# Kernel tuning notes

Measured on AMD Instinct MI355X. Metric: run time of the kernel, lower is better.

## Reference

```python
import jax, jax.numpy as jnp
import numpy as np

T = 4096          # total tokens across ragged segments
H = 4096          # hidden_size
I = 11008         # intermediate_size
R = 16            # lora_rank
A = 4             # number of adapters (segments)


def setup_inputs() -> dict:
    key = jax.random.key(0)
    ks = jax.random.split(key, 12)
    inp = {
        "x": jax.random.normal(ks[0], (T, H), jnp.float32),
        "gate_w": jax.random.normal(ks[1], (I, H), jnp.float32) * (1.0 / np.sqrt(H)),
        "up_w": jax.random.normal(ks[2], (I, H), jnp.float32) * (1.0 / np.sqrt(H)),
        "down_w": jax.random.normal(ks[3], (H, I), jnp.float32) * (1.0 / np.sqrt(I)),
        "gate_wa": jax.random.normal(ks[4], (A, H, R), jnp.float32) * 0.01,
        "gate_wb": jax.random.normal(ks[5], (A, R, I), jnp.float32) * 0.01,
        "up_wa": jax.random.normal(ks[6], (A, H, R), jnp.float32) * 0.01,
        "up_wb": jax.random.normal(ks[7], (A, R, I), jnp.float32) * 0.01,
        "down_wa": jax.random.normal(ks[8], (A, I, R), jnp.float32) * 0.01,
        "down_wb": jax.random.normal(ks[9], (A, R, H), jnp.float32) * 0.01,
        "seg_ids": jnp.sort(jax.random.randint(ks[10], (T,), 0, A, jnp.int32)),
    }
    return inp


def _add_lora(y, inp, wa, wb, mask):
    # Segment-batched low-rank GEMM (Punica/S-LoRA add_lora):
    # for token t in segment a:  y[t] += inp[t] @ wa[a] @ wb[a]
    # mask: [T, A] one-hot of token->adapter assignment.
    # [A, T, R]: project into rank space for every adapter (R tiny), mask out
    xa = jnp.einsum('th,ahr->tar', inp, wa) * mask[:, :, None]   # [T, A, R]
    a, r = wb.shape[0], wb.shape[1]
    # collapse (A, R) so the expansion is one GEMM, no [A, T, out] intermediate
    delta = xa.reshape(inp.shape[0], a * r) @ wb.reshape(a * r, wb.shape[2])
    return y + delta


def reference(x, gate_w, up_w, down_w, gate_wa, gate_wb, up_wa, up_wb,
              down_wa, down_wb, seg_ids):
    mask = (seg_ids[:, None] == jnp.arange(A, dtype=seg_ids.dtype)[None, :]
            ).astype(x.dtype)                                    # [T, A]
    gate = x @ gate_w.T                                          # [T, I]
    gate = _add_lora(gate, x, gate_wa, gate_wb, mask)
    gate = jax.nn.silu(gate)
    up = x @ up_w.T                                              # [T, I]
    up = _add_lora(up, x, up_wa, up_wb, mask)
    t = gate * up
    down = t @ down_w.T                                          # [T, H]
    down = _add_lora(down, t, down_wa, down_wb, mask)
    return down
```

## Files before the change

kernel.cpp:

```cpp
#include <hip/hip_runtime.h>

#define T_TOK 4096
#define HID   4096
#define IMD   11008

using f32x4  = __attribute__((ext_vector_type(4))) float;
using bf16x8 = __attribute__((ext_vector_type(8))) __bf16;
union FragCast { int4 i; bf16x8 b; };

__device__ __forceinline__ unsigned f2bf_bits(float f) {
  unsigned u = __float_as_uint(f);
  return (u + 0x7fffu + ((u >> 16) & 1u)) >> 16;
}
__device__ __forceinline__ float bf2f(short s) {
  return __uint_as_float(((unsigned)(unsigned short)s) << 16);
}
__device__ __forceinline__ int4 cvt8(const float4 f0, const float4 f1) {
  int4 r;
  r.x = f2bf_bits(f0.x) | (f2bf_bits(f0.y) << 16);
  r.y = f2bf_bits(f0.z) | (f2bf_bits(f0.w) << 16);
  r.z = f2bf_bits(f1.x) | (f2bf_bits(f1.y) << 16);
  r.w = f2bf_bits(f1.z) | (f2bf_bits(f1.w) << 16);
  return r;
}
__device__ __forceinline__ void gload16(const void* g, void* l) {
  __builtin_amdgcn_global_load_lds(
      (__attribute__((address_space(1))) void*)g,
      (__attribute__((address_space(3))) void*)l, 16, 0, 0);
}

__global__ void cvt_pad(const float* __restrict__ in, short* __restrict__ out,
                        int C8, long ldin, long ldout) {
  long r = blockIdx.x;
  const float4* s = (const float4*)(in + r * ldin);
  int4* d = (int4*)(out + r * ldout);
  for (int c = threadIdx.x; c < C8; c += blockDim.x)
    d[c] = cvt8(s[2 * c], s[2 * c + 1]);
}

__global__ void build_wbT_pad(const float* __restrict__ wb,
                              short* __restrict__ out, int N, long ldout,
                              long K) {
  int n = blockIdx.x * blockDim.x + threadIdx.x;
  int ar = blockIdx.y;
  if (n < N) out[(long)n * ldout + K + ar] = (short)f2bf_bits(wb[(long)ar * N + n]);
}

__global__ void tail_copy(const short* __restrict__ src, short* dst, long ld) {
  dst[(long)blockIdx.x * ld + threadIdx.x] = src[blockIdx.x * 64 + threadIdx.x];
}

template <int KD, int NOUT>
__global__ __launch_bounds__(256)
void lora_proj(const short* __restrict__ Abf, long ldA,
               const float* __restrict__ wa0, const float* __restrict__ wa1,
               const int* __restrict__ seg, short* out0, long ld0, short* out1,
               long ld1) {
  __shared__ __align__(16) short rowbuf[KD];
  __shared__ float part[NOUT][4][16];
  int t = blockIdx.x, tid = threadIdx.x;
  int a = seg[t];
  const int4* src = (const int4*)(Abf + (long)t * ldA);
  for (int c = tid; c < KD / 8; c += 256) ((int4*)rowbuf)[c] = src[c];
  __syncthreads();
  int w = tid >> 6, l = tid & 63;
  int r = l & 15, g = l >> 4;
  const int HW = KD / 4;
  float s0 = 0.f, s1 = 0.f;
  const float* p0 = wa0 + (long)a * KD * 16 + r;
  const float* p1 = (NOUT == 2) ? (wa1 + (long)a * KD * 16 + r) : nullptr;
  int h = w * HW + g;
  for (int k = 0; k < HW / 4; ++k, h += 4) {
    float xv = bf2f(rowbuf[h]);
    s0 = fmaf(xv, p0[(long)h * 16], s0);
    if (NOUT == 2) s1 = fmaf(xv, p1[(long)h * 16], s1);
  }
  s0 += __shfl_xor(s0, 16); s0 += __shfl_xor(s0, 32);
  if (NOUT == 2) { s1 += __shfl_xor(s1, 16); s1 += __shfl_xor(s1, 32); }
  if (l < 16) { part[0][w][r] = s0; if (NOUT == 2) part[1][w][r] = s1; }
  __syncthreads();
  if (tid < 64 * NOUT) {
    int m = tid >> 6, ar = tid & 63;
    float v = 0.f;
    if ((ar >> 4) == a) {
      int r2 = ar & 15;
      v = part[m][0][r2] + part[m][1][r2] + part[m][2][r2] + part[m][3][r2];
    }
    short b = (short)f2bf_bits(v);
    if (m == 0) out0[(long)t * ld0 + ar] = b;
    else        out1[(long)t * ld1 + ar] = b;
  }
}

template <int MODE>
__global__ __launch_bounds__(512, 2)
void gemm256(const short* __restrict__ A, const short* __restrict__ B,
             const short* gbuf, short* outB, float* outF, int nby, long ldK,
             int iters, long ldo) {
  extern __shared__ __align__(16) char smem[];

  int nwg = gridDim.x;
  int orig = blockIdx.x;
  int q = nwg >> 3, rr = nwg & 7;
  int xcd = orig & 7, loc = orig >> 3;
  int swz = (xcd < rr ? xcd * (q + 1) : rr * (q + 1) + (xcd - rr) * q) + loc;
  int by = swz % nby, bx = swz / nby;
  long row0 = (long)bx * 256, col0 = (long)by * 256;

  int tid = threadIdx.x;
  int l = tid & 63, wid = tid >> 6;
  int wr = wid >> 2, wc = wid & 3;
  int lrow = l & 15, lhi = l >> 4, md = lrow & 7;

  const short* aP[4]; const short* bP[4];
  int dst[4];
#pragma unroll
  for (int k = 0; k < 4; ++k) {
    int idx = tid + k * 512;
    int r = idx >> 3, c8 = idx & 7;
    aP[k] = A + (row0 + r) * ldK + (c8 ^ (r & 7)) * 8;
    bP[k] = B + (col0 + r) * ldK + (c8 ^ (r & 7)) * 8;
    dst[k] = idx * 16;
  }

  auto stageA = [&](int bi) {
    char* d = smem + bi * 32768;
#pragma unroll
    for (int k = 0; k < 4; ++k) { gload16(aP[k], d + dst[k]); aP[k] += 64; }
  };
  auto stageB = [&](int bi) {
    char* d = smem + 98304 + bi * 32768;
#pragma unroll
    for (int k = 0; k < 4; ++k) { gload16(bP[k], d + dst[k]); bP[k] += 64; }
  };

  f32x4 acc[8][4];
  f32x4 zr = {0.f, 0.f, 0.f, 0.f};
#pragma unroll
  for (int mi = 0; mi < 8; ++mi)
#pragma unroll
    for (int ni = 0; ni < 4; ++ni) acc[mi][ni] = zr;

  const int csel0 = (lhi ^ md) * 16;
  const int csel1 = ((4 + lhi) ^ md) * 16;

  stageA(0); stageB(0); stageA(1);
  int ca = 0, sa = 2;
  for (int t = 0; t < iters; ++t) {
    if (t + 1 < iters) asm volatile("s_waitcnt vmcnt(4)" ::: "memory");
    else               asm volatile("s_waitcnt vmcnt(0)" ::: "memory");
    asm volatile("s_barrier" ::: "memory");
    if (t + 1 < iters) stageB((t + 1) & 1);
    if (t + 2 < iters) { stageA(sa); sa = (sa == 2) ? 0 : sa + 1; }

    const char* Ab = smem + ca * 32768;
    const char* Bb = smem + 98304 + (t & 1) * 32768;
    ca = (ca == 2) ? 0 : ca + 1;

    bf16x8 bF[4][2];
#pragma unroll
    for (int ni = 0; ni < 4; ++ni) {
      const char* base = Bb + (wc * 64 + ni * 16 + lrow) * 128;
      FragCast f0, f1;
      f0.i = *(const int4*)(base + csel0);
      f1.i = *(const int4*)(base + csel1);
      bF[ni][0] = f0.b; bF[ni][1] = f1.b;
    }
#pragma unroll
    for (int qm = 0; qm < 2; ++qm) {
      bf16x8 aF[4][2];
#pragma unroll
      for (int mi = 0; mi < 4; ++mi) {
        const char* base = Ab + (wr * 128 + qm * 64 + mi * 16 + lrow) * 128;
        FragCast f0, f1;
        f0.i = *(const int4*)(base + csel0);
        f1.i = *(const int4*)(base + csel1);
        aF[mi][0] = f0.b; aF[mi][1] = f1.b;
      }
      __builtin_amdgcn_s_setprio(1);
#pragma unroll
      for (int mi = 0; mi < 4; ++mi)
#pragma unroll
        for (int ni = 0; ni < 4; ++ni) {
          acc[qm * 4 + mi][ni] = __builtin_amdgcn_mfma_f32_16x16x32_bf16(
              aF[mi][0], bF[ni][0], acc[qm * 4 + mi][ni], 0, 0, 0);
          acc[qm * 4 + mi][ni] = __builtin_amdgcn_mfma_f32_16x16x32_bf16(
              aF[mi][1], bF[ni][1], acc[qm * 4 + mi][ni], 0, 0, 0);
        }
      __builtin_amdgcn_s_setprio(0);
    }
  }

#pragma unroll
  for (int qm = 0; qm < 2; ++qm)
#pragma unroll
    for (int mi = 0; mi < 4; ++mi)
#pragma unroll
      for (int ni = 0; ni < 4; ++ni)
#pragma unroll
        for (int j = 0; j < 4; ++j) {
          long grow = row0 + wr * 128 + qm * 64 + mi * 16 + lhi * 4 + j;
          long gcol = col0 + wc * 64 + ni * 16 + lrow;
          long idx = grow * ldo + gcol;
          float v = acc[qm * 4 + mi][ni][j];
          if constexpr (MODE == 0) {
            outB[idx] = (short)f2bf_bits(v);
          } else if constexpr (MODE == 1) {
            float g = bf2f(gbuf[idx]);
            float t2 = g * (1.f / (1.f + __expf(-g))) * v;
            outB[idx] = (short)f2bf_bits(t2);
          } else {
            outF[idx] = v;
          }
        }
}

extern "C" void kernel_launch(void* const* d_in, const int* in_sizes, int n_in,
                              void* d_out, int out_size, void* d_ws,
                              size_t ws_size, hipStream_t stream) {
  const float* x       = (const float*)d_in[0];
  const float* gate_w  = (const float*)d_in[1];
  const float* up_w    = (const float*)d_in[2];
  const float* down_w  = (const float*)d_in[3];
  const float* gate_wa = (const float*)d_in[4];
  const float* gate_wb = (const float*)d_in[5];
  const float* up_wa   = (const float*)d_in[6];
  const float* up_wb   = (const float*)d_in[7];
  const float* down_wa = (const float*)d_in[8];
  const float* down_wb = (const float*)d_in[9];
  const int*   seg     = (const int*)d_in[10];

  char* ws = (char*)d_ws;
  short* xg_pad = (short*)(ws);
  short* wA     = (short*)(ws + 34078720);
  short* wB     = (short*)(ws + 125665280);
  short* t_pad  = (short*)(ws + 217251840);
  short* xa_u   = (short*)(ws + 307953664);

  const int LDS_BYTES = 163840;
  hipFuncSetAttribute(reinterpret_cast<const void*>(&gemm256<0>),
                      hipFuncAttributeMaxDynamicSharedMemorySize, LDS_BYTES);
  hipFuncSetAttribute(reinterpret_cast<const void*>(&gemm256<1>),
                      hipFuncAttributeMaxDynamicSharedMemorySize, LDS_BYTES);
  hipFuncSetAttribute(reinterpret_cast<const void*>(&gemm256<2>),
                      hipFuncAttributeMaxDynamicSharedMemorySize, LDS_BYTES);

  cvt_pad<<<T_TOK, 256, 0, stream>>>(x, xg_pad, 512, HID, 4160);
  cvt_pad<<<IMD, 256, 0, stream>>>(gate_w, wA, 512, HID, 4160);
  cvt_pad<<<IMD, 256, 0, stream>>>(up_w, wB, 512, HID, 4160);
  build_wbT_pad<<<dim3(43, 64), 256, 0, stream>>>(gate_wb, wA, IMD, 4160, HID);
  build_wbT_pad<<<dim3(43, 64), 256, 0, stream>>>(up_wb, wB, IMD, 4160, HID);
  lora_proj<HID, 2><<<T_TOK, 256, 0, stream>>>(
      xg_pad, 4160, gate_wa, up_wa, seg, xg_pad + HID, 4160, xa_u, 64);

  gemm256<0><<<16 * 43, 512, LDS_BYTES, stream>>>(
      xg_pad, wA, nullptr, t_pad, nullptr, 43, 4160, 65, 11072);
  tail_copy<<<T_TOK, 64, 0, stream>>>(xa_u, xg_pad + HID, 4160);
  gemm256<1><<<16 * 43, 512, LDS_BYTES, stream>>>(
      xg_pad, wB, t_pad, t_pad, nullptr, 43, 4160, 65, 11072);

  cvt_pad<<<T_TOK, 256, 0, stream>>>(down_w, wA, 1376, IMD, 11072);
  build_wbT_pad<<<dim3(16, 64), 256, 0, stream>>>(down_wb, wA, HID, 11072, IMD);
  lora_proj<IMD, 1><<<T_TOK, 256, 0, stream>>>(
      t_pad, 11072, down_wa, nullptr, seg, t_pad + IMD, 11072, nullptr, 64);

  gemm256<2><<<16 * 16, 512, LDS_BYTES, stream>>>(
      t_pad, wA, nullptr, nullptr, (float*)d_out, 16, 11072, 173, 4096);
}
```

Baseline: 1.719 ms.

## Interleave global-to-LDS stage loads across four MFMA phases per K-step

Each K-iteration of the GEMM main loop is split into four phases, each handling 32 rows of the A tile. Half-tile global loads for the next B and next-next A buffers are issued between these phases, instead of all at once at the top of the iteration. Barriers are placed around each MFMA cluster so waves stay in lockstep, in the style of ping-pong scheduling. The aim is to spread memory issue across the compute and keep the MFMA pipe busy. The cost is eight barriers per iteration instead of one, which may add stalls.

```diff
diff --git a/kernel.cpp b/kernel.cpp
--- a/kernel.cpp
+++ b/kernel.cpp
@@ -123,15 +123,15 @@
     dst[k] = idx * 16;
   }
 
-  auto stageA = [&](int bi) {
+  auto stageA_h = [&](int bi, int h) {
     char* d = smem + bi * 32768;
-#pragma unroll
-    for (int k = 0; k < 4; ++k) { gload16(aP[k], d + dst[k]); aP[k] += 64; }
+    gload16(aP[2 * h], d + dst[2 * h]);         aP[2 * h] += 64;
+    gload16(aP[2 * h + 1], d + dst[2 * h + 1]); aP[2 * h + 1] += 64;
   };
-  auto stageB = [&](int bi) {
+  auto stageB_h = [&](int bi, int h) {
     char* d = smem + 98304 + bi * 32768;
-#pragma unroll
-    for (int k = 0; k < 4; ++k) { gload16(bP[k], d + dst[k]); bP[k] += 64; }
+    gload16(bP[2 * h], d + dst[2 * h]);         bP[2 * h] += 64;
+    gload16(bP[2 * h + 1], d + dst[2 * h + 1]); bP[2 * h + 1] += 64;
   };
 
   f32x4 acc[8][4];
@@ -144,75 +144,88 @@
   const int csel0 = (lhi ^ md) * 16;
   const int csel1 = ((4 + lhi) ^ md) * 16;
 
-  stageA(0); stageB(0); stageA(1);
-  int ca = 0, sa = 2;
+  stageA_h(0, 0); stageA_h(0, 1);
+  stageB_h(0, 0); stageB_h(0, 1);
+  stageA_h(1, 0); stageA_h(1, 1);
+  asm volatile("s_waitcnt vmcnt(4)" ::: "memory");
+  asm volatile("s_barrier" ::: "memory");
+
+  int ca = 0;
   for (int t = 0; t < iters; ++t) {
-    if (t + 1 < iters) asm volatile("s_waitcnt vmcnt(4)" ::: "memory");
-    else               asm volatile("s_waitcnt vmcnt(0)" ::: "memory");
-    asm volatile("s_barrier" ::: "memory");
-    if (t + 1 < iters) stageB((t + 1) & 1);
-    if (t + 2 < iters) { stageA(sa); sa = (sa == 2) ? 0 : sa + 1; }
-
     const char* Ab = smem + ca * 32768;
     const char* Bb = smem + 98304 + (t & 1) * 32768;
-    ca = (ca == 2) ? 0 : ca + 1;
-
+    int na2 = (ca >= 1) ? ca - 1 : 2;
+    int nb1 = (t + 1) & 1;
     bf16x8 bF[4][2];
-#pragma unroll
-    for (int ni = 0; ni < 4; ++ni) {
-      const char* base = Bb + (wc * 64 + ni * 16 + lrow) * 128;
-      FragCast f0, f1;
-      f0.i = *(const int4*)(base + csel0);
-      f1.i = *(const int4*)(base + csel1);
-      bF[ni][0] = f0.b; bF[ni][1] = f1.b;
-    }
-#pragma unroll
-    for (int qm = 0; qm < 2; ++qm) {
-      bf16x8 aF[4][2];
-#pragma unroll
-      for (int mi = 0; mi < 4; ++mi) {
-        const char* base = Ab + (wr * 128 + qm * 64 + mi * 16 + lrow) * 128;
+
+#pragma unroll
+    for (int p = 0; p < 4; ++p) {
+      if (p == 0) {
+#pragma unroll
+        for (int ni = 0; ni < 4; ++ni) {
+          const char* base = Bb + (wc * 64 + ni * 16 + lrow) * 128;
+          FragCast f0, f1;
+          f0.i = *(const int4*)(base + csel0);
+          f1.i = *(const int4*)(base + csel1);
+          bF[ni][0] = f0.b; bF[ni][1] = f1.b;
+        }
+      }
+      bf16x8 aF[2][2];
+#pragma unroll
+      for (int m2 = 0; m2 < 2; ++m2) {
+        const char* base = Ab + (wr * 128 + p * 32 + m2 * 16 + lrow) * 128;
         FragCast f0, f1;
         f0.i = *(const int4*)(base + csel0);
         f1.i = *(const int4*)(base + csel1);
-        aF[mi][0] = f0.b; aF[mi][1] = f1.b;
-      }
+        aF[m2][0] = f0.b; aF[m2][1] = f1.b;
+      }
+      if (p == 0 && t + 1 < iters) stageB_h(nb1, 0);
+      if (p == 1 && t + 1 < iters) stageB_h(nb1, 1);
+      if (p == 2 && t + 2 < iters) stageA_h(na2, 0);
+      if (p == 3) {
+        if (t + 2 < iters) {
+          stageA_h(na2, 1);
+          asm volatile("s_waitcnt vmcnt(4)" ::: "memory");
+        } else {
+          asm volatile("s_waitcnt vmcnt(0)" ::: "memory");
+        }
+      }
+      asm volatile("s_barrier" ::: "memory");
       __builtin_amdgcn_s_setprio(1);
 #pragma unroll
-      for (int mi = 0; mi < 4; ++mi)
-#pragma unroll
-        for (int ni = 0; ni < 4; ++ni) {
-          acc[qm * 4 + mi][ni] = __builtin_amdgcn_mfma_f32_16x16x32_bf16(
-              aF[mi][0], bF[ni][0], acc[qm * 4 + mi][ni], 0, 0, 0);
-          acc[qm * 4 + mi][ni] = __builtin_amdgcn_mfma_f32_16x16x32_bf16(
-              aF[mi][1], bF[ni][1], acc[qm * 4 + mi][ni], 0, 0, 0);
+      for (int k = 0; k < 2; ++k)
+#pragma unroll
+        for (int m2 = 0; m2 < 2; ++m2)
+#pragma unroll
+          for (int ni = 0; ni < 4; ++ni)
+            acc[p * 2 + m2][ni] = __builtin_amdgcn_mfma_f32_16x16x32_bf16(
+                aF[m2][k], bF[ni][k], acc[p * 2 + m2][ni], 0, 0, 0);
+      __builtin_amdgcn_s_setprio(0);
+      asm volatile("s_barrier" ::: "memory");
+    }
+    ca = (ca == 2) ? 0 : ca + 1;
+  }
+
+#pragma unroll
+  for (int mi = 0; mi < 8; ++mi)
+#pragma unroll
+    for (int ni = 0; ni < 4; ++ni)
+#pragma unroll
+      for (int j = 0; j < 4; ++j) {
+        long grow = row0 + wr * 128 + mi * 16 + lhi * 4 + j;
+        long gcol = col0 + wc * 64 + ni * 16 + lrow;
+        long idx = grow * ldo + gcol;
+        float v = acc[mi][ni][j];
+        if constexpr (MODE == 0) {
+          outB[idx] = (short)f2bf_bits(v);
+        } else if constexpr (MODE == 1) {
+          float g = bf2f(gbuf[idx]);
+          float t2 = g * (1.f / (1.f + __expf(-g))) * v;
+          outB[idx] = (short)f2bf_bits(t2);
+        } else {
+          outF[idx] = v;
         }
-      __builtin_amdgcn_s_setprio(0);
-    }
-  }
-
-#pragma unroll
-  for (int qm = 0; qm < 2; ++qm)
-#pragma unroll
-    for (int mi = 0; mi < 4; ++mi)
-#pragma unroll
-      for (int ni = 0; ni < 4; ++ni)
-#pragma unroll
-        for (int j = 0; j < 4; ++j) {
-          long grow = row0 + wr * 128 + qm * 64 + mi * 16 + lhi * 4 + j;
-          long gcol = col0 + wc * 64 + ni * 16 + lrow;
-          long idx = grow * ldo + gcol;
-          float v = acc[qm * 4 + mi][ni][j];
-          if constexpr (MODE == 0) {
-            outB[idx] = (short)f2bf_bits(v);
-          } else if constexpr (MODE == 1) {
-            float g = bf2f(gbuf[idx]);
-            float t2 = g * (1.f / (1.f + __expf(-g))) * v;
-            outB[idx] = (short)f2bf_bits(t2);
-          } else {
-            outF[idx] = v;
-          }
-        }
+      }
 }
 
 extern "C" void kernel_launch(void* const* d_in, const int* in_sizes, int n_in,
```

After: 1.679 ms. 1.02x faster.

## Restructure GEMM mainloop into 8-phase ping-pong schedule with half-tile staging

Applied to the files above, without the earlier changes.

Replaces the triple-buffered A / double-buffered B mainloop with a two-buffer ping-pong schedule. Each K-tile is split into half-tile loads interleaved with quarter-tile MFMA blocks, separated by barriers, in the style of hipBLASLt 8-wave schedules. The aim is finer-grained overlap of global loads, LDS reads and MFMA work, and LDS use drops from 160KB to 128KB. The cost is many more barriers per iteration and a more fragile pipeline; odd-NT handling relies on a tail step that assumes NT is odd (65 and 173 are).

```diff
diff --git a/kernel.cpp b/kernel.cpp
--- a/kernel.cpp
+++ b/kernel.cpp
@@ -94,10 +94,11 @@
 
 template <int MODE>
 __global__ __launch_bounds__(512, 2)
-void gemm256(const short* __restrict__ A, const short* __restrict__ B,
-             const short* gbuf, short* outB, float* outF, int nby, long ldK,
-             int iters, long ldo) {
+void gemm8p(const short* __restrict__ A, const short* __restrict__ B,
+            const short* gbuf, short* outB, float* outF, int nby, long ldK,
+            int NT, long ldo) {
   extern __shared__ __align__(16) char smem[];
+  const int D1 = 65536;
 
   int nwg = gridDim.x;
   int orig = blockIdx.x;
@@ -112,26 +113,21 @@
   int wr = wid >> 2, wc = wid & 3;
   int lrow = l & 15, lhi = l >> 4, md = lrow & 7;
 
-  const short* aP[4]; const short* bP[4];
-  int dst[4];
-#pragma unroll
-  for (int k = 0; k < 4; ++k) {
-    int idx = tid + k * 512;
-    int r = idx >> 3, c8 = idx & 7;
-    aP[k] = A + (row0 + r) * ldK + (c8 ^ (r & 7)) * 8;
-    bP[k] = B + (col0 + r) * ldK + (c8 ^ (r & 7)) * 8;
-    dst[k] = idx * 16;
-  }
-
-  auto stageA = [&](int bi) {
-    char* d = smem + bi * 32768;
-#pragma unroll
-    for (int k = 0; k < 4; ++k) { gload16(aP[k], d + dst[k]); aP[k] += 64; }
-  };
-  auto stageB = [&](int bi) {
-    char* d = smem + 98304 + bi * 32768;
-#pragma unroll
-    for (int k = 0; k < 4; ++k) { gload16(bP[k], d + dst[k]); bP[k] += 64; }
+  const int rr0 = tid >> 3, cc0 = tid & 7;
+  const short* pA0 = A + (row0 + rr0) * ldK + (cc0 ^ (rr0 & 7)) * 8;
+  const short* pB0 = B + (col0 + rr0) * ldK + (cc0 ^ (rr0 & 7)) * 8;
+
+  auto stA = [&](int db, int hh, int kt) {
+    const short* s = pA0 + (long)hh * 128 * ldK + (long)kt * 64;
+    char* d = smem + db + hh * 16384 + tid * 16;
+    gload16(s, d);
+    gload16(s + 64 * ldK, d + 8192);
+  };
+  auto stB = [&](int db, int hh, int kt) {
+    const short* s = pB0 + (long)hh * 128 * ldK + (long)kt * 64;
+    char* d = smem + db + 32768 + hh * 16384 + tid * 16;
+    gload16(s, d);
+    gload16(s + 64 * ldK, d + 8192);
   };
 
   f32x4 acc[8][4];
@@ -141,78 +137,129 @@
 #pragma unroll
     for (int ni = 0; ni < 4; ++ni) acc[mi][ni] = zr;
 
-  const int csel0 = (lhi ^ md) * 16;
-  const int csel1 = ((4 + lhi) ^ md) * 16;
-
-  stageA(0); stageB(0); stageA(1);
-  int ca = 0, sa = 2;
-  for (int t = 0; t < iters; ++t) {
-    if (t + 1 < iters) asm volatile("s_waitcnt vmcnt(4)" ::: "memory");
-    else               asm volatile("s_waitcnt vmcnt(0)" ::: "memory");
-    asm volatile("s_barrier" ::: "memory");
-    if (t + 1 < iters) stageB((t + 1) & 1);
-    if (t + 2 < iters) { stageA(sa); sa = (sa == 2) ? 0 : sa + 1; }
-
-    const char* Ab = smem + ca * 32768;
-    const char* Bb = smem + 98304 + (t & 1) * 32768;
-    ca = (ca == 2) ? 0 : ca + 1;
-
-    bf16x8 bF[4][2];
-#pragma unroll
-    for (int ni = 0; ni < 4; ++ni) {
-      const char* base = Bb + (wc * 64 + ni * 16 + lrow) * 128;
-      FragCast f0, f1;
-      f0.i = *(const int4*)(base + csel0);
-      f1.i = *(const int4*)(base + csel1);
-      bF[ni][0] = f0.b; bF[ni][1] = f1.b;
+  bf16x8 aF[4][2], bQ0[2][2], bQ1[2][2];
+
+  auto readA = [&](int db, int qm) {
+#pragma unroll
+    for (int mi = 0; mi < 4; ++mi) {
+      const char* p = smem + db + wr * 16384 + (qm * 64 + mi * 16 + lrow) * 128;
+#pragma unroll
+      for (int k = 0; k < 2; ++k) {
+        FragCast f; f.i = *(const int4*)(p + ((k * 4 + lhi) ^ md) * 16);
+        aF[mi][k] = f.b;
+      }
     }
-#pragma unroll
-    for (int qm = 0; qm < 2; ++qm) {
-      bf16x8 aF[4][2];
-#pragma unroll
-      for (int mi = 0; mi < 4; ++mi) {
-        const char* base = Ab + (wr * 128 + qm * 64 + mi * 16 + lrow) * 128;
-        FragCast f0, f1;
-        f0.i = *(const int4*)(base + csel0);
-        f1.i = *(const int4*)(base + csel1);
-        aF[mi][0] = f0.b; aF[mi][1] = f1.b;
+  };
+  auto readB = [&](int db, int qn, bf16x8 (&bq)[2][2]) {
+#pragma unroll
+    for (int nj = 0; nj < 2; ++nj) {
+      const char* p = smem + db + 32768 + (wc >> 1) * 16384 +
+                      ((wc & 1) * 64 + qn * 32 + nj * 16 + lrow) * 128;
+#pragma unroll
+      for (int k = 0; k < 2; ++k) {
+        FragCast f; f.i = *(const int4*)(p + ((k * 4 + lhi) ^ md) * 16);
+        bq[nj][k] = f.b;
       }
-      __builtin_amdgcn_s_setprio(1);
+    }
+  };
+  auto mfma16 = [&](int qm, int qn, bf16x8 (&bq)[2][2]) {
+    __builtin_amdgcn_s_setprio(1);
+#pragma unroll
+    for (int k = 0; k < 2; ++k)
 #pragma unroll
       for (int mi = 0; mi < 4; ++mi)
 #pragma unroll
-        for (int ni = 0; ni < 4; ++ni) {
-          acc[qm * 4 + mi][ni] = __builtin_amdgcn_mfma_f32_16x16x32_bf16(
-              aF[mi][0], bF[ni][0], acc[qm * 4 + mi][ni], 0, 0, 0);
-          acc[qm * 4 + mi][ni] = __builtin_amdgcn_mfma_f32_16x16x32_bf16(
-              aF[mi][1], bF[ni][1], acc[qm * 4 + mi][ni], 0, 0, 0);
+        for (int nj = 0; nj < 2; ++nj)
+          acc[qm * 4 + mi][qn * 2 + nj] =
+              __builtin_amdgcn_mfma_f32_16x16x32_bf16(
+                  aF[mi][k], bq[nj][k], acc[qm * 4 + mi][qn * 2 + nj], 0, 0, 0);
+    __builtin_amdgcn_s_setprio(0);
+  };
+
+  stA(0, 0, 0); stA(0, 1, 0); stB(0, 0, 0); stB(0, 1, 0);
+  stB(D1, 0, 1); stB(D1, 1, 1);
+  asm volatile("s_waitcnt vmcnt(4)" ::: "memory");
+  __builtin_amdgcn_s_barrier();
+
+  const int NI = (NT - 1) >> 1;
+#pragma unroll 1
+  for (int i = 0; i < NI; ++i) {
+    const int t2 = 2 * i;
+    const bool so = (t2 + 3) < NT;
+    readA(0, 0); readB(0, 0, bQ0);
+    stA(D1, 0, t2 + 1);
+    __builtin_amdgcn_s_barrier();
+    mfma16(0, 0, bQ0);
+    __builtin_amdgcn_s_barrier();
+    readB(0, 1, bQ1);
+    stA(D1, 1, t2 + 1);
+    __builtin_amdgcn_s_barrier();
+    mfma16(0, 1, bQ1);
+    __builtin_amdgcn_s_barrier();
+    readA(0, 1);
+    stB(0, 0, t2 + 2);
+    __builtin_amdgcn_s_barrier();
+    mfma16(1, 1, bQ1);
+    __builtin_amdgcn_s_barrier();
+    stB(0, 1, t2 + 2);
+    asm volatile("s_waitcnt vmcnt(4)" ::: "memory");
+    __builtin_amdgcn_s_barrier();
+    mfma16(1, 0, bQ0);
+    __builtin_amdgcn_s_barrier();
+    readA(D1, 0); readB(D1, 0, bQ0);
+    stA(0, 0, t2 + 2);
+    __builtin_amdgcn_s_barrier();
+    mfma16(0, 0, bQ0);
+    __builtin_amdgcn_s_barrier();
+    readB(D1, 1, bQ1);
+    stA(0, 1, t2 + 2);
+    __builtin_amdgcn_s_barrier();
+    mfma16(0, 1, bQ1);
+    __builtin_amdgcn_s_barrier();
+    readA(D1, 1);
+    if (so) stB(D1, 0, t2 + 3);
+    __builtin_amdgcn_s_barrier();
+    mfma16(1, 1, bQ1);
+    __builtin_amdgcn_s_barrier();
+    if (so) {
+      stB(D1, 1, t2 + 3);
+      asm volatile("s_waitcnt vmcnt(4)" ::: "memory");
+    } else {
+      asm volatile("s_waitcnt vmcnt(0)" ::: "memory");
+    }
+    __builtin_amdgcn_s_barrier();
+    mfma16(1, 0, bQ0);
+    __builtin_amdgcn_s_barrier();
+  }
+
+  readA(0, 0); readB(0, 0, bQ0); readB(0, 1, bQ1);
+  mfma16(0, 0, bQ0);
+  mfma16(0, 1, bQ1);
+  readA(0, 1);
+  mfma16(1, 1, bQ1);
+  mfma16(1, 0, bQ0);
+
+#pragma unroll
+  for (int mi = 0; mi < 8; ++mi)
+#pragma unroll
+    for (int ni = 0; ni < 4; ++ni)
+#pragma unroll
+      for (int j = 0; j < 4; ++j) {
+        long grow = row0 + wr * 128 + (mi >> 2) * 64 + (mi & 3) * 16 +
+                    lhi * 4 + j;
+        long gcol = col0 + wc * 64 + ni * 16 + lrow;
+        long idx = grow * ldo + gcol;
+        float v = acc[mi][ni][j];
+        if constexpr (MODE == 0) {
+          outB[idx] = (short)f2bf_bits(v);
+        } else if constexpr (MODE == 1) {
+          float g = bf2f(gbuf[idx]);
+          float t2 = g * (1.f / (1.f + __expf(-g))) * v;
+          outB[idx] = (short)f2bf_bits(t2);
+        } else {
+          outF[idx] = v;
         }
-      __builtin_amdgcn_s_setprio(0);
-    }
-  }
-
-#pragma unroll
-  for (int qm = 0; qm < 2; ++qm)
-#pragma unroll
-    for (int mi = 0; mi < 4; ++mi)
-#pragma unroll
-      for (int ni = 0; ni < 4; ++ni)
-#pragma unroll
-        for (int j = 0; j < 4; ++j) {
-          long grow = row0 + wr * 128 + qm * 64 + mi * 16 + lhi * 4 + j;
-          long gcol = col0 + wc * 64 + ni * 16 + lrow;
-          long idx = grow * ldo + gcol;
-          float v = acc[qm * 4 + mi][ni][j];
-          if constexpr (MODE == 0) {
-            outB[idx] = (short)f2bf_bits(v);
-          } else if constexpr (MODE == 1) {
-            float g = bf2f(gbuf[idx]);
-            float t2 = g * (1.f / (1.f + __expf(-g))) * v;
-            outB[idx] = (short)f2bf_bits(t2);
-          } else {
-            outF[idx] = v;
-          }
-        }
+      }
 }
 
 extern "C" void kernel_launch(void* const* d_in, const int* in_sizes, int n_in,
@@ -237,12 +284,12 @@
   short* t_pad  = (short*)(ws + 217251840);
   short* xa_u   = (short*)(ws + 307953664);
 
-  const int LDS_BYTES = 163840;
-  hipFuncSetAttribute(reinterpret_cast<const void*>(&gemm256<0>),
+  const int LDS_BYTES = 131072;
+  hipFuncSetAttribute(reinterpret_cast<const void*>(&gemm8p<0>),
                       hipFuncAttributeMaxDynamicSharedMemorySize, LDS_BYTES);
-  hipFuncSetAttribute(reinterpret_cast<const void*>(&gemm256<1>),
+  hipFuncSetAttribute(reinterpret_cast<const void*>(&gemm8p<1>),
                       hipFuncAttributeMaxDynamicSharedMemorySize, LDS_BYTES);
-  hipFuncSetAttribute(reinterpret_cast<const void*>(&gemm256<2>),
+  hipFuncSetAttribute(reinterpret_cast<const void*>(&gemm8p<2>),
                       hipFuncAttributeMaxDynamicSharedMemorySize, LDS_BYTES);
 
   cvt_pad<<<T_TOK, 256, 0, stream>>>(x, xg_pad, 512, HID, 4160);
@@ -253,10 +300,10 @@
   lora_proj<HID, 2><<<T_TOK, 256, 0, stream>>>(
       xg_pad, 4160, gate_wa, up_wa, seg, xg_pad + HID, 4160, xa_u, 64);
 
-  gemm256<0><<<16 * 43, 512, LDS_BYTES, stream>>>(
+  gemm8p<0><<<16 * 43, 512, LDS_BYTES, stream>>>(
       xg_pad, wA, nullptr, t_pad, nullptr, 43, 4160, 65, 11072);
   tail_copy<<<T_TOK, 64, 0, stream>>>(xa_u, xg_pad + HID, 4160);
-  gemm256<1><<<16 * 43, 512, LDS_BYTES, stream>>>(
+  gemm8p<1><<<16 * 43, 512, LDS_BYTES, stream>>>(
       xg_pad, wB, t_pad, t_pad, nullptr, 43, 4160, 65, 11072);
 
   cvt_pad<<<T_TOK, 256, 0, stream>>>(down_w, wA, 1376, IMD, 11072);
@@ -264,6 +311,6 @@
   lora_proj<IMD, 1><<<T_TOK, 256, 0, stream>>>(
       t_pad, 11072, down_wa, nullptr, seg, t_pad + IMD, 11072, nullptr, 64);
 
-  gemm256<2><<<16 * 16, 512, LDS_BYTES, stream>>>(
+  gemm8p<2><<<16 * 16, 512, LDS_BYTES, stream>>>(
       t_pad, wA, nullptr, nullptr, (float*)d_out, 16, 11072, 173, 4096);
 }
```

Measured after the change: 1.855 ms. 1.08x slower.

## Replace gate and down GEMMs with simple 128x128 single-buffered MFMA kernel

Applied to the files above, without the earlier changes.

Adds a simpler 128x128-tile bf16 MFMA GEMM with 256 threads, static LDS and a single-stage load/compute loop, and uses it for the gate and down projections in place of the 256x256 double-LDS kernel. The up projection still uses the large kernel. The smaller tiles give more workgroups and better occupancy, but they cut data reuse per tile, add a sync pair every K step with no overlap of load and compute, and write the epilogue with scalar stores.

```diff
diff --git a/kernel.cpp b/kernel.cpp
--- a/kernel.cpp
+++ b/kernel.cpp
@@ -93,6 +93,93 @@
 }
 
 template <int MODE>
+__global__ __launch_bounds__(256)
+void gemm97(const short* __restrict__ A, const short* __restrict__ B,
+            const short* __restrict__ gbuf, short* __restrict__ outB,
+            float* __restrict__ outF, int nbx, long ldK, int iters, long ldo) {
+  __shared__ __align__(16) short sA[128 * 32];
+  __shared__ __align__(16) short sB[128 * 32];
+
+  int nwg = gridDim.x;
+  int orig = blockIdx.x;
+  int q = nwg >> 3, rr = nwg & 7;
+  int xcd = orig & 7, loc = orig >> 3;
+  int swz = (xcd < rr ? xcd * (q + 1) : rr * (q + 1) + (xcd - rr) * q) + loc;
+  int bx = swz % nbx, by = swz / nbx;
+  long row0 = (long)bx * 128, col0 = (long)by * 128;
+
+  int tid = threadIdx.x;
+  int l = tid & 63, wid = tid >> 6;
+  int wr = wid >> 1, wc = wid & 1;
+  int lrow = l & 15, lhi = l >> 4;
+
+  int r0 = tid >> 2, k0 = (tid & 3) * 8;
+  const short* aS0 = A + (row0 + r0) * ldK + k0;
+  const short* aS1 = A + (row0 + r0 + 64) * ldK + k0;
+  const short* bS0 = B + (col0 + r0) * ldK + k0;
+  const short* bS1 = B + (col0 + r0 + 64) * ldK + k0;
+  char* dA0 = (char*)sA + tid * 16; char* dA1 = dA0 + 4096;
+  char* dB0 = (char*)sB + tid * 16; char* dB1 = dB0 + 4096;
+
+  f32x4 acc[4][4];
+  f32x4 zr = {0.f, 0.f, 0.f, 0.f};
+#pragma unroll
+  for (int mi = 0; mi < 4; ++mi)
+#pragma unroll
+    for (int ni = 0; ni < 4; ++ni) acc[mi][ni] = zr;
+
+  const int aOff = wr * 4096 + lrow * 64 + lhi * 16;
+  const int bOff = wc * 4096 + lrow * 64 + lhi * 16;
+
+#pragma unroll 1
+  for (int it = 0; it < iters; ++it) {
+    __syncthreads();
+    gload16(aS0, dA0); gload16(aS1, dA1);
+    gload16(bS0, dB0); gload16(bS1, dB1);
+    aS0 += 32; aS1 += 32; bS0 += 32; bS1 += 32;
+    __syncthreads();
+    bf16x8 aF[4], bF[4];
+#pragma unroll
+    for (int mi = 0; mi < 4; ++mi) {
+      FragCast f; f.i = *(const int4*)((const char*)sA + aOff + mi * 1024);
+      aF[mi] = f.b;
+    }
+#pragma unroll
+    for (int ni = 0; ni < 4; ++ni) {
+      FragCast f; f.i = *(const int4*)((const char*)sB + bOff + ni * 1024);
+      bF[ni] = f.b;
+    }
+#pragma unroll
+    for (int mi = 0; mi < 4; ++mi)
+#pragma unroll
+      for (int ni = 0; ni < 4; ++ni)
+        acc[mi][ni] = __builtin_amdgcn_mfma_f32_16x16x32_bf16(
+            aF[mi], bF[ni], acc[mi][ni], 0, 0, 0);
+  }
+
+#pragma unroll
+  for (int mi = 0; mi < 4; ++mi)
+#pragma unroll
+    for (int ni = 0; ni < 4; ++ni)
+#pragma unroll
+      for (int j = 0; j < 4; ++j) {
+        long grow = row0 + wr * 64 + mi * 16 + lhi * 4 + j;
+        long gcol = col0 + wc * 64 + ni * 16 + lrow;
+        long idx = grow * ldo + gcol;
+        float v = acc[mi][ni][j];
+        if constexpr (MODE == 0) {
+          outB[idx] = (short)f2bf_bits(v);
+        } else if constexpr (MODE == 1) {
+          float g = bf2f(gbuf[idx]);
+          float t2 = g * (1.f / (1.f + __expf(-g))) * v;
+          outB[idx] = (short)f2bf_bits(t2);
+        } else {
+          outF[idx] = v;
+        }
+      }
+}
+
+template <int MODE>
 __global__ __launch_bounds__(512, 2)
 void gemm256(const short* __restrict__ A, const short* __restrict__ B,
              const short* gbuf, short* outB, float* outF, int nby, long ldK,
@@ -238,11 +325,7 @@
   short* xa_u   = (short*)(ws + 307953664);
 
   const int LDS_BYTES = 163840;
-  hipFuncSetAttribute(reinterpret_cast<const void*>(&gemm256<0>),
-                      hipFuncAttributeMaxDynamicSharedMemorySize, LDS_BYTES);
   hipFuncSetAttribute(reinterpret_cast<const void*>(&gemm256<1>),
-                      hipFuncAttributeMaxDynamicSharedMemorySize, LDS_BYTES);
-  hipFuncSetAttribute(reinterpret_cast<const void*>(&gemm256<2>),
                       hipFuncAttributeMaxDynamicSharedMemorySize, LDS_BYTES);
 
   cvt_pad<<<T_TOK, 256, 0, stream>>>(x, xg_pad, 512, HID, 4160);
@@ -253,8 +336,9 @@
   lora_proj<HID, 2><<<T_TOK, 256, 0, stream>>>(
       xg_pad, 4160, gate_wa, up_wa, seg, xg_pad + HID, 4160, xa_u, 64);
 
-  gemm256<0><<<16 * 43, 512, LDS_BYTES, stream>>>(
-      xg_pad, wA, nullptr, t_pad, nullptr, 43, 4160, 65, 11072);
+  gemm97<0><<<32 * 86, 256, 0, stream>>>(
+      xg_pad, wA, nullptr, t_pad, nullptr, 32, 4160, 130, 11072);
+
   tail_copy<<<T_TOK, 64, 0, stream>>>(xa_u, xg_pad + HID, 4160);
   gemm256<1><<<16 * 43, 512, LDS_BYTES, stream>>>(
       xg_pad, wB, t_pad, t_pad, nullptr, 43, 4160, 65, 11072);
@@ -264,6 +348,6 @@
   lora_proj<IMD, 1><<<T_TOK, 256, 0, stream>>>(
       t_pad, 11072, down_wa, nullptr, seg, t_pad + IMD, 11072, nullptr, 64);
 
-  gemm256<2><<<16 * 16, 512, LDS_BYTES, stream>>>(
-      t_pad, wA, nullptr, nullptr, (float*)d_out, 16, 11072, 173, 4096);
-}
+  gemm97<2><<<32 * 32, 256, 0, stream>>>(
+      t_pad, wA, nullptr, nullptr, (float*)d_out, 32, 11072, 346, 4096);
+}
```

Result: slower. 1.953 ms (+13.6%).
